# Optimization experiments

Hardware: AMD Instinct MI355X
Metric: run time of the kernel (lower is better)

The kernel has to match this reference:

```python
import jax, jax.numpy as jnp
import numpy as np
from jax import lax

# norse LIF/LI default parameters
DT = 0.001
TAU_SYN_INV = 200.0   # 1/5e-3
TAU_MEM_INV = 100.0   # 1/1e-2
V_TH = 1.0
V_LEAK = 0.0
V_RESET = 0.0
ALPHA = 100.0         # SuperSpike surrogate slope (method='super')
SEQ_LEN = 40          # LIFConstantCurrentEncoder(40)
SCALE = 50.0

@jax.custom_vjp
def heaviside(x):
    # forward: spike if x > 0; backward: SuperSpike surrogate
    return (x > 0).astype(x.dtype)

def _h_fwd(x):
    return (x > 0).astype(x.dtype), x

def _h_bwd(x, g):
    return (g / (ALPHA * jnp.abs(x) + 1.0) ** 2,)

heaviside.defvjp(_h_fwd, _h_bwd)

def constant_current_encode(current):
    # LIF membrane driven by a constant input current; emit spike train (T, B, F)
    def step(v, _):
        v = v + DT * TAU_MEM_INV * ((V_LEAK - v) + current)
        z = heaviside(v - V_TH)
        v = (1.0 - z) * v  # reset to zero on spike
        return v, z
    _, spikes = lax.scan(step, jnp.zeros_like(current), None, length=SEQ_LEN)
    return spikes

def setup_inputs() -> dict:
    key = jax.random.key(0)
    k1, k2, k3, k4 = jax.random.split(key, 4)
    batch, state_dim, hidden, out = 65536, 4, 128, 2
    x = jax.random.normal(k1, (batch, state_dim), jnp.float32)
    s_in = np.float32(np.sqrt(1.0 / (2 * state_dim)))
    s_hid = np.float32(np.sqrt(1.0 / hidden))
    w_in = jax.random.normal(k2, (hidden, 2 * state_dim), jnp.float32) * s_in   # LIFCell input weights
    w_rec = jax.random.normal(k3, (hidden, hidden), jnp.float32) * s_hid        # LIFCell recurrent weights
    w_out = jax.random.normal(k4, (out, hidden), jnp.float32) * s_hid           # LICell readout weights
    return {"x": x, "w_in": w_in, "w_rec": w_rec, "w_out": w_out}

def reference(x, w_in, w_rec, w_out):
    # encode positive / negative parts of the (scaled) observation into spikes
    x_pos = constant_current_encode(jax.nn.relu(SCALE * x))   # (T, B, 4)
    x_neg = constant_current_encode(jax.nn.relu(-SCALE * x))  # (T, B, 4)
    spikes = jnp.concatenate([x_pos, x_neg], axis=2)          # (T, B, 8)

    B = x.shape[0]
    H = w_in.shape[0]
    O = w_out.shape[0]
    z0 = jnp.zeros((B, H), x.dtype)
    v0 = jnp.zeros((B, H), x.dtype)
    i0 = jnp.zeros((B, H), x.dtype)
    vo0 = jnp.zeros((B, O), x.dtype)
    io0 = jnp.zeros((B, O), x.dtype)

    def step(carry, xt):
        z, v, i, vo, io = carry
        # --- LIFCell (recurrent spiking layer) ---
        i_dec = i - DT * TAU_SYN_INV * i
        v_dec = v + DT * TAU_MEM_INV * ((V_LEAK - v) + i)
        z_new = heaviside(v_dec - V_TH)
        v_new = (1.0 - z_new) * v_dec + z_new * V_RESET
        i_new = i_dec + xt @ w_in.T + z @ w_rec.T
        # dropout(p=0.5) is identity in eval mode
        # --- LICell (leaky-integrator readout) ---
        vo_new = vo + DT * TAU_MEM_INV * ((V_LEAK - vo) + io)
        io_new = io - DT * TAU_SYN_INV * io + z_new @ w_out.T
        return (z_new, v_new, i_new, vo_new, io_new), vo_new

    _, voltages = lax.scan(step, (z0, v0, i0, vo0, io0), spikes)  # (T, B, 2)
    m = jnp.max(voltages, axis=0)
    return jax.nn.softmax(m, axis=1)
```

## Files before the change

### kernel.cpp

```cpp
#include <hip/hip_runtime.h>


#pragma clang fp contract(off)

typedef float f32x4 __attribute__((ext_vector_type(4)));
typedef float f32x2 __attribute__((ext_vector_type(2)));
typedef short short8 __attribute__((ext_vector_type(8)));
typedef int int4v __attribute__((ext_vector_type(4)));

constexpr int TSTEPS = 40;

__device__ __forceinline__ unsigned rnbf(float f) {
    unsigned u = __float_as_uint(f);
    return (u + 0x7FFFu + ((u >> 16) & 1u)) & 0xFFFF0000u;
}

__device__ __forceinline__ void split2pair(float a, float b,
                                           unsigned& hi, unsigned& mi) {
    unsigned ha = rnbf(a), hb = rnbf(b);
    float ra = a - __uint_as_float(ha);
    float rb = b - __uint_as_float(hb);
    unsigned ma = rnbf(ra), mb = rnbf(rb);
    hi = (ha >> 16) | (hb & 0xFFFF0000u);
    mi = (ma >> 16) | (mb & 0xFFFF0000u);
}

__device__ __forceinline__ f32x4 mfma16(int4v a, int4v b, f32x4 c) {
    return __builtin_amdgcn_mfma_f32_16x16x32_bf16(
        __builtin_bit_cast(short8, a), __builtin_bit_cast(short8, b), c, 0, 0, 0);
}

template <int CTRL>
__device__ __forceinline__ float dpp_mov(float v) {
    return __int_as_float(
        __builtin_amdgcn_update_dpp(0, __float_as_int(v), CTRL, 0xF, 0xF, true));
}

__device__ __forceinline__ f32x2 lo2(f32x4 a) {
    return __builtin_shufflevector(a, a, 0, 1);
}
__device__ __forceinline__ f32x2 hi2(f32x4 a) {
    return __builtin_shufflevector(a, a, 2, 3);
}

__global__ __launch_bounds__(256, 3) void snn_kernel(
    const float* __restrict__ x,
    const float* __restrict__ w_in,
    const float* __restrict__ w_rec,
    const float* __restrict__ w_out,
    float* __restrict__ out)
{
    __shared__ char zraw[8192];

    const int tid = threadIdx.x;
    const int l   = tid & 63;
    const int wv  = tid >> 6;
    const int cl  = l & 15;
    const int kg  = l >> 4;
    const int kb  = kg * 8;
    const int b0  = blockIdx.x * 16;
    const int Ns  = wv * 32;

    const f32x2 P1  = {0.1f, 0.1f};
    const f32x2 P02 = {0.2f, 0.2f};

    int4v BrecHi[2][4], BrecMi[2][4];
#pragma unroll
    for (int t = 0; t < 2; ++t) {
        int n = Ns + t * 16 + cl;
#pragma unroll
        for (int kc = 0; kc < 4; ++kc) {
            const float* wp = w_rec + n * 128 + kc * 32 + kb;
            float4 wa = *reinterpret_cast<const float4*>(wp);
            float4 wb = *reinterpret_cast<const float4*>(wp + 4);
            float w8[8] = {wa.x, wa.y, wa.z, wa.w, wb.x, wb.y, wb.z, wb.w};
#pragma unroll
            for (int r = 0; r < 4; ++r) {
                unsigned h, m;
                split2pair(w8[2 * r], w8[2 * r + 1], h, m);
                BrecHi[t][kc][r] = (int)h;
                BrecMi[t][kc][r] = (int)m;
            }
        }
    }

    int4v BwinPk[2];
#pragma unroll
    for (int t = 0; t < 2; ++t) {
        int n = Ns + t * 16 + cl;
        float w8[8];
#pragma unroll
        for (int j = 0; j < 8; ++j)
            w8[j] = (kg < 2) ? w_in[n * 8 + j] : 0.0f;
#pragma unroll
        for (int r = 0; r < 4; ++r) {
            unsigned h, m;
            split2pair(w8[2 * r], w8[2 * r + 1], h, m);
            BwinPk[t][r] = (int)(kg == 0 ? h : (kg == 1 ? m : 0u));
        }
    }

    int4v Bwout[4];
    {
        int  ch   = cl & 1;
        int  part = (cl >> 1) & 1;
        bool act  = cl < 4;
#pragma unroll
        for (int kc = 0; kc < 4; ++kc) {
            float w8[8];
#pragma unroll
            for (int j = 0; j < 8; ++j)
                w8[j] = act ? w_out[ch * 128 + kc * 32 + kb + j] : 0.0f;
#pragma unroll
            for (int r = 0; r < 4; ++r) {
                unsigned h, m;
                split2pair(w8[2 * r], w8[2 * r + 1], h, m);
                Bwout[kc][r] = (int)(part ? m : h);
            }
        }
    }

    float xv0 = x[(size_t)(b0 + (l >> 3)) * 4 + (l & 3)];
    float xv1 = x[(size_t)(b0 + 8 + (l >> 3)) * 4 + (l & 3)];
    float s0 = 50.0f * xv0, s1 = 50.0f * xv1;
    f32x2 cur;
    cur[0] = (l & 4) ? fmaxf(-s0, 0.0f) : fmaxf(s0, 0.0f);
    cur[1] = (l & 4) ? fmaxf(-s1, 0.0f) : fmaxf(s1, 0.0f);
    f32x2 ve = {0.0f, 0.0f};

    f32x2 iSl[2] = {{0,0},{0,0}}, iSh[2] = {{0,0},{0,0}};
    f32x2 vSl[2] = {{0,0},{0,0}}, vSh[2] = {{0,0},{0,0}};
    f32x2 io_l = {0,0}, io_h = {0,0}, vo_l = {0,0}, vo_h = {0,0};
    f32x4 mx = {-3e38f,-3e38f,-3e38f,-3e38f};

    unsigned awrb[2];
#pragma unroll
    for (int t = 0; t < 2; ++t) {
        int col = Ns + t * 16 + cl;
        awrb[t] = (unsigned)((kg * 1024 + col * 2) ^ ((kg & 1) << 6));
    }
    unsigned ard = (unsigned)((cl * 256 + kg * 16) ^ ((cl & 7) << 4)) | 4096u;

    auto loadfrags = [&](int4v* zf) {
#pragma unroll
        for (int kc = 0; kc < 4; ++kc)
            zf[kc] = *reinterpret_cast<int4v*>(&zraw[ard ^ (unsigned)(kc << 6)]);
    };

    auto readout = [&](const int4v* zf) {
        f32x4 cro = {0,0,0,0};
#pragma unroll
        for (int kc = 0; kc < 4; ++kc) cro = mfma16(zf[kc], Bwout[kc], cro);
        f32x4 cr;
#pragma unroll
        for (int r = 0; r < 4; ++r) cr[r] = cro[r] + dpp_mov<0x4E>(cro[r]);
        f32x2 t2l = io_l - vo_l;
        f32x2 t2h = io_h - vo_h;
        f32x2 vnl = vo_l + P1 * t2l;
        f32x2 vnh = vo_h + P1 * t2h;
        io_l = (io_l - P02 * io_l) + lo2(cr);
        io_h = (io_h - P02 * io_h) + hi2(cr);
        vo_l = vnl;
        vo_h = vnh;
        mx[0] = fmaxf(mx[0], vnl[0]);
        mx[1] = fmaxf(mx[1], vnl[1]);
        mx[2] = fmaxf(mx[2], vnh[0]);
        mx[3] = fmaxf(mx[3], vnh[1]);
    };

    auto encoder_lif = [&](bool with_rec, const int4v* zf) {
        f32x2 te = cur - ve;
        f32x2 vv = ve + P1 * te;
        bool e0 = vv[0] > 1.0f, e1 = vv[1] > 1.0f;
        unsigned long long bm0 = __ballot(e0), bm1 = __ballot(e1);
        ve[0] = e0 ? 0.0f : vv[0];
        ve[1] = e1 ? 0.0f : vv[1];
        unsigned long long src = (cl < 8) ? (bm0 >> (cl * 8)) : (bm1 >> ((cl - 8) * 8));
        unsigned byt = (l < 32) ? ((unsigned)src & 0xFFu) : 0u;
        int4v axt;
        axt[0] = (int)(((byt & 1u)   ? 0x3F80u : 0u) | ((byt & 2u)   ? 0x3F800000u : 0u));
        axt[1] = (int)(((byt & 4u)   ? 0x3F80u : 0u) | ((byt & 8u)   ? 0x3F800000u : 0u));
        axt[2] = (int)(((byt & 16u)  ? 0x3F80u : 0u) | ((byt & 32u)  ? 0x3F800000u : 0u));
        axt[3] = (int)(((byt & 64u)  ? 0x3F80u : 0u) | ((byt & 128u) ? 0x3F800000u : 0u));
#pragma unroll
        for (int t = 0; t < 2; ++t) {
            f32x4 cin = {0,0,0,0};
            cin = mfma16(axt, BwinPk[t], cin);
            f32x4 crec = {0,0,0,0};
            if (with_rec) {
#pragma unroll
                for (int kc = 0; kc < 4; ++kc)
                    crec = mfma16(zf[kc], BrecMi[t][kc], crec);
#pragma unroll
                for (int kc = 0; kc < 4; ++kc)
                    crec = mfma16(zf[kc], BrecHi[t][kc], crec);
            }
            f32x2 idl = iSl[t] - P02 * iSl[t];
            f32x2 idh = iSh[t] - P02 * iSh[t];
            f32x2 ttl = iSl[t] - vSl[t];
            f32x2 tth = iSh[t] - vSh[t];
            f32x2 vdl = vSl[t] + P1 * ttl;
            f32x2 vdh = vSh[t] + P1 * tth;
#pragma unroll
            for (int r = 0; r < 4; ++r) {
                float vdr = (r < 2) ? vdl[r] : vdh[r - 2];
                bool zb = vdr > 1.0f;
                float vres = zb ? 0.0f : vdr;
                if (r == 0)      vSl[t][0] = vres;
                else if (r == 1) vSl[t][1] = vres;
                else if (r == 2) vSh[t][0] = vres;
                else             vSh[t][1] = vres;
                short zv = zb ? (short)0x3F80 : (short)0;
                unsigned a = (awrb[t] ^ (unsigned)(r << 4)) + (unsigned)(r * 256);
                *reinterpret_cast<short*>(&zraw[a]) = zv;
            }
            iSl[t] = (idl + lo2(cin)) + lo2(crec);
            iSh[t] = (idh + hi2(cin)) + hi2(crec);
        }
    };

    auto toggle = [&]() {
        ard ^= 4096u;
        awrb[0] ^= 4096u;
        awrb[1] ^= 4096u;
    };

    encoder_lif(false, nullptr);
    __syncthreads();
    toggle();

#pragma unroll 1
    for (int u = 1; u < TSTEPS; ++u) {
        int4v zf[4];
        loadfrags(zf);
        readout(zf);
        encoder_lif(true, zf);
        __syncthreads();
        toggle();
    }

    {
        int4v zf[4];
        loadfrags(zf);
        readout(zf);
    }

#pragma unroll
    for (int r = 0; r < 4; ++r) {
        float partner = dpp_mov<0xB1>(mx[r]);
        float mm = fmaxf(mx[r], partner);
        float es = expf(mx[r] - mm);
        float ep = expf(partner - mm);
        float inv = 1.0f / (es + ep);
        float pr = es * inv;
        if (cl < 2) out[(size_t)(b0 + kg * 4 + r) * 2 + cl] = pr;
    }
}

extern "C" void kernel_launch(void* const* d_in, const int* in_sizes, int n_in,
                              void* d_out, int out_size, void* d_ws, size_t ws_size,
                              hipStream_t stream) {
    const float* x     = (const float*)d_in[0];
    const float* w_in  = (const float*)d_in[1];
    const float* w_rec = (const float*)d_in[2];
    const float* w_out = (const float*)d_in[3];
    float* out = (float*)d_out;

    int B = in_sizes[0] / 4;
    int blocks = B / 16;
    snn_kernel<<<blocks, 256, 0, stream>>>(x, w_in, w_rec, w_out, out);
}
```

Baseline: 266.5 us.

## Process two independent batch tiles per block to interleave dependent MFMA chains

Each block now handles 32 batch rows as two independent 16-row tiles (A and B) whose recurrent MFMA chains, LIF updates and readouts are interleaved in the same loop. The shared spike buffer doubles and the grid halves. This gives the scheduler independent work to hide MFMA and LDS latency, and halves the number of barriers and weight-splitting preambles per row. In exchange, register pressure roughly doubles for state, and launch bounds drop to two blocks per CU, reducing occupancy.

Result: slower. 277.4 us (+4.1%).

```diff
diff --git a/kernel.cpp b/kernel.cpp
--- a/kernel.cpp
+++ b/kernel.cpp
@@ -43,14 +43,14 @@
     return __builtin_shufflevector(a, a, 2, 3);
 }
 
-__global__ __launch_bounds__(256, 3) void snn_kernel(
+__global__ __launch_bounds__(256, 2) void snn_kernel(
     const float* __restrict__ x,
     const float* __restrict__ w_in,
     const float* __restrict__ w_rec,
     const float* __restrict__ w_out,
     float* __restrict__ out)
 {
-    __shared__ char zraw[8192];
+    __shared__ char zraw[16384];
 
     const int tid = threadIdx.x;
     const int l   = tid & 63;
@@ -58,7 +58,7 @@
     const int cl  = l & 15;
     const int kg  = l >> 4;
     const int kb  = kg * 8;
-    const int b0  = blockIdx.x * 16;
+    const int b0  = blockIdx.x * 32;
     const int Ns  = wv * 32;
 
     const f32x2 P1  = {0.1f, 0.1f};
@@ -122,16 +122,25 @@
 
     float xv0 = x[(size_t)(b0 + (l >> 3)) * 4 + (l & 3)];
     float xv1 = x[(size_t)(b0 + 8 + (l >> 3)) * 4 + (l & 3)];
+    float xv2 = x[(size_t)(b0 + 16 + (l >> 3)) * 4 + (l & 3)];
+    float xv3 = x[(size_t)(b0 + 24 + (l >> 3)) * 4 + (l & 3)];
     float s0 = 50.0f * xv0, s1 = 50.0f * xv1;
-    f32x2 cur;
-    cur[0] = (l & 4) ? fmaxf(-s0, 0.0f) : fmaxf(s0, 0.0f);
-    cur[1] = (l & 4) ? fmaxf(-s1, 0.0f) : fmaxf(s1, 0.0f);
-    f32x2 ve = {0.0f, 0.0f};
-
-    f32x2 iSl[2] = {{0,0},{0,0}}, iSh[2] = {{0,0},{0,0}};
-    f32x2 vSl[2] = {{0,0},{0,0}}, vSh[2] = {{0,0},{0,0}};
-    f32x2 io_l = {0,0}, io_h = {0,0}, vo_l = {0,0}, vo_h = {0,0};
-    f32x4 mx = {-3e38f,-3e38f,-3e38f,-3e38f};
+    float s2 = 50.0f * xv2, s3 = 50.0f * xv3;
+    f32x2 curA, curB;
+    curA[0] = (l & 4) ? fmaxf(-s0, 0.0f) : fmaxf(s0, 0.0f);
+    curA[1] = (l & 4) ? fmaxf(-s1, 0.0f) : fmaxf(s1, 0.0f);
+    curB[0] = (l & 4) ? fmaxf(-s2, 0.0f) : fmaxf(s2, 0.0f);
+    curB[1] = (l & 4) ? fmaxf(-s3, 0.0f) : fmaxf(s3, 0.0f);
+    f32x2 veA = {0.0f, 0.0f}, veB = {0.0f, 0.0f};
+
+    f32x2 iSlA[2] = {{0,0},{0,0}}, iShA[2] = {{0,0},{0,0}};
+    f32x2 vSlA[2] = {{0,0},{0,0}}, vShA[2] = {{0,0},{0,0}};
+    f32x2 iSlB[2] = {{0,0},{0,0}}, iShB[2] = {{0,0},{0,0}};
+    f32x2 vSlB[2] = {{0,0},{0,0}}, vShB[2] = {{0,0},{0,0}};
+    f32x2 ioA_l = {0,0}, ioA_h = {0,0}, voA_l = {0,0}, voA_h = {0,0};
+    f32x2 ioB_l = {0,0}, ioB_h = {0,0}, voB_l = {0,0}, voB_h = {0,0};
+    f32x4 mxA = {-3e38f,-3e38f,-3e38f,-3e38f};
+    f32x4 mxB = {-3e38f,-3e38f,-3e38f,-3e38f};
 
     unsigned awrb[2];
 #pragma unroll
@@ -139,42 +148,61 @@
         int col = Ns + t * 16 + cl;
         awrb[t] = (unsigned)((kg * 1024 + col * 2) ^ ((kg & 1) << 6));
     }
-    unsigned ard = (unsigned)((cl * 256 + kg * 16) ^ ((cl & 7) << 4)) | 4096u;
-
-    auto loadfrags = [&](int4v* zf) {
-#pragma unroll
-        for (int kc = 0; kc < 4; ++kc)
-            zf[kc] = *reinterpret_cast<int4v*>(&zraw[ard ^ (unsigned)(kc << 6)]);
-    };
-
-    auto readout = [&](const int4v* zf) {
-        f32x4 cro = {0,0,0,0};
-#pragma unroll
-        for (int kc = 0; kc < 4; ++kc) cro = mfma16(zf[kc], Bwout[kc], cro);
-        f32x4 cr;
-#pragma unroll
-        for (int r = 0; r < 4; ++r) cr[r] = cro[r] + dpp_mov<0x4E>(cro[r]);
-        f32x2 t2l = io_l - vo_l;
-        f32x2 t2h = io_h - vo_h;
-        f32x2 vnl = vo_l + P1 * t2l;
-        f32x2 vnh = vo_h + P1 * t2h;
-        io_l = (io_l - P02 * io_l) + lo2(cr);
-        io_h = (io_h - P02 * io_h) + hi2(cr);
-        vo_l = vnl;
-        vo_h = vnh;
-        mx[0] = fmaxf(mx[0], vnl[0]);
-        mx[1] = fmaxf(mx[1], vnl[1]);
-        mx[2] = fmaxf(mx[2], vnh[0]);
-        mx[3] = fmaxf(mx[3], vnh[1]);
-    };
-
-    auto encoder_lif = [&](bool with_rec, const int4v* zf) {
-        f32x2 te = cur - ve;
-        f32x2 vv = ve + P1 * te;
-        bool e0 = vv[0] > 1.0f, e1 = vv[1] > 1.0f;
-        unsigned long long bm0 = __ballot(e0), bm1 = __ballot(e1);
-        ve[0] = e0 ? 0.0f : vv[0];
-        ve[1] = e1 ? 0.0f : vv[1];
+    unsigned ard = (unsigned)((cl * 256 + kg * 16) ^ ((cl & 7) << 4)) | 8192u;
+
+    auto loadfrags = [&](int4v* zfA, int4v* zfB) {
+#pragma unroll
+        for (int kc = 0; kc < 4; ++kc) {
+            unsigned a = ard ^ (unsigned)(kc << 6);
+            zfA[kc] = *reinterpret_cast<int4v*>(&zraw[a]);
+            zfB[kc] = *reinterpret_cast<int4v*>(&zraw[a ^ 4096u]);
+        }
+    };
+
+    auto readout = [&](const int4v* zfA, const int4v* zfB) {
+        f32x4 croA = {0,0,0,0}, croB = {0,0,0,0};
+#pragma unroll
+        for (int kc = 0; kc < 4; ++kc) {
+            croA = mfma16(zfA[kc], Bwout[kc], croA);
+            croB = mfma16(zfB[kc], Bwout[kc], croB);
+        }
+        f32x4 crA, crB;
+#pragma unroll
+        for (int r = 0; r < 4; ++r) {
+            crA[r] = croA[r] + dpp_mov<0x4E>(croA[r]);
+            crB[r] = croB[r] + dpp_mov<0x4E>(croB[r]);
+        }
+        {
+            f32x2 t2l = ioA_l - voA_l;
+            f32x2 t2h = ioA_h - voA_h;
+            f32x2 vnl = voA_l + P1 * t2l;
+            f32x2 vnh = voA_h + P1 * t2h;
+            ioA_l = (ioA_l - P02 * ioA_l) + lo2(crA);
+            ioA_h = (ioA_h - P02 * ioA_h) + hi2(crA);
+            voA_l = vnl;
+            voA_h = vnh;
+            mxA[0] = fmaxf(mxA[0], vnl[0]);
+            mxA[1] = fmaxf(mxA[1], vnl[1]);
+            mxA[2] = fmaxf(mxA[2], vnh[0]);
+            mxA[3] = fmaxf(mxA[3], vnh[1]);
+        }
+        {
+            f32x2 t2l = ioB_l - voB_l;
+            f32x2 t2h = ioB_h - voB_h;
+            f32x2 vnl = voB_l + P1 * t2l;
+            f32x2 vnh = voB_h + P1 * t2h;
+            ioB_l = (ioB_l - P02 * ioB_l) + lo2(crB);
+            ioB_h = (ioB_h - P02 * ioB_h) + hi2(crB);
+            voB_l = vnl;
+            voB_h = vnh;
+            mxB[0] = fmaxf(mxB[0], vnl[0]);
+            mxB[1] = fmaxf(mxB[1], vnl[1]);
+            mxB[2] = fmaxf(mxB[2], vnh[0]);
+            mxB[3] = fmaxf(mxB[3], vnh[1]);
+        }
+    };
+
+    auto make_axt = [&](unsigned long long bm0, unsigned long long bm1) {
         unsigned long long src = (cl < 8) ? (bm0 >> (cl * 8)) : (bm1 >> ((cl - 8) * 8));
         unsigned byt = (l < 32) ? ((unsigned)src & 0xFFu) : 0u;
         int4v axt;
@@ -182,78 +210,135 @@
         axt[1] = (int)(((byt & 4u)   ? 0x3F80u : 0u) | ((byt & 8u)   ? 0x3F800000u : 0u));
         axt[2] = (int)(((byt & 16u)  ? 0x3F80u : 0u) | ((byt & 32u)  ? 0x3F800000u : 0u));
         axt[3] = (int)(((byt & 64u)  ? 0x3F80u : 0u) | ((byt & 128u) ? 0x3F800000u : 0u));
+        return axt;
+    };
+
+    auto encoder_lif = [&](bool with_rec, const int4v* zfA, const int4v* zfB) {
+        f32x2 teA = curA - veA;
+        f32x2 vvA = veA + P1 * teA;
+        f32x2 teB = curB - veB;
+        f32x2 vvB = veB + P1 * teB;
+        bool e0 = vvA[0] > 1.0f, e1 = vvA[1] > 1.0f;
+        bool e2 = vvB[0] > 1.0f, e3 = vvB[1] > 1.0f;
+        unsigned long long bm0A = __ballot(e0), bm1A = __ballot(e1);
+        unsigned long long bm0B = __ballot(e2), bm1B = __ballot(e3);
+        veA[0] = e0 ? 0.0f : vvA[0];
+        veA[1] = e1 ? 0.0f : vvA[1];
+        veB[0] = e2 ? 0.0f : vvB[0];
+        veB[1] = e3 ? 0.0f : vvB[1];
+        int4v axtA = make_axt(bm0A, bm1A);
+        int4v axtB = make_axt(bm0B, bm1B);
 #pragma unroll
         for (int t = 0; t < 2; ++t) {
-            f32x4 cin = {0,0,0,0};
-            cin = mfma16(axt, BwinPk[t], cin);
-            f32x4 crec = {0,0,0,0};
+            f32x4 cinA = {0,0,0,0}, cinB = {0,0,0,0};
+            cinA = mfma16(axtA, BwinPk[t], cinA);
+            cinB = mfma16(axtB, BwinPk[t], cinB);
+            f32x4 crecA = {0,0,0,0}, crecB = {0,0,0,0};
             if (with_rec) {
 #pragma unroll
-                for (int kc = 0; kc < 4; ++kc)
-                    crec = mfma16(zf[kc], BrecMi[t][kc], crec);
-#pragma unroll
-                for (int kc = 0; kc < 4; ++kc)
-                    crec = mfma16(zf[kc], BrecHi[t][kc], crec);
-            }
-            f32x2 idl = iSl[t] - P02 * iSl[t];
-            f32x2 idh = iSh[t] - P02 * iSh[t];
-            f32x2 ttl = iSl[t] - vSl[t];
-            f32x2 tth = iSh[t] - vSh[t];
-            f32x2 vdl = vSl[t] + P1 * ttl;
-            f32x2 vdh = vSh[t] + P1 * tth;
-#pragma unroll
-            for (int r = 0; r < 4; ++r) {
-                float vdr = (r < 2) ? vdl[r] : vdh[r - 2];
-                bool zb = vdr > 1.0f;
-                float vres = zb ? 0.0f : vdr;
-                if (r == 0)      vSl[t][0] = vres;
-                else if (r == 1) vSl[t][1] = vres;
-                else if (r == 2) vSh[t][0] = vres;
-                else             vSh[t][1] = vres;
-                short zv = zb ? (short)0x3F80 : (short)0;
-                unsigned a = (awrb[t] ^ (unsigned)(r << 4)) + (unsigned)(r * 256);
-                *reinterpret_cast<short*>(&zraw[a]) = zv;
-            }
-            iSl[t] = (idl + lo2(cin)) + lo2(crec);
-            iSh[t] = (idh + hi2(cin)) + hi2(crec);
+                for (int kc = 0; kc < 4; ++kc) {
+                    crecA = mfma16(zfA[kc], BrecMi[t][kc], crecA);
+                    crecB = mfma16(zfB[kc], BrecMi[t][kc], crecB);
+                }
+#pragma unroll
+                for (int kc = 0; kc < 4; ++kc) {
+                    crecA = mfma16(zfA[kc], BrecHi[t][kc], crecA);
+                    crecB = mfma16(zfB[kc], BrecHi[t][kc], crecB);
+                }
+            }
+            {
+                f32x2 idl = iSlA[t] - P02 * iSlA[t];
+                f32x2 idh = iShA[t] - P02 * iShA[t];
+                f32x2 ttl = iSlA[t] - vSlA[t];
+                f32x2 tth = iShA[t] - vShA[t];
+                f32x2 vdl = vSlA[t] + P1 * ttl;
+                f32x2 vdh = vShA[t] + P1 * tth;
+#pragma unroll
+                for (int r = 0; r < 4; ++r) {
+                    float vdr = (r < 2) ? vdl[r] : vdh[r - 2];
+                    bool zb = vdr > 1.0f;
+                    float vres = zb ? 0.0f : vdr;
+                    if (r == 0)      vSlA[t][0] = vres;
+                    else if (r == 1) vSlA[t][1] = vres;
+                    else if (r == 2) vShA[t][0] = vres;
+                    else             vShA[t][1] = vres;
+                    short zv = zb ? (short)0x3F80 : (short)0;
+                    unsigned a = (awrb[t] ^ (unsigned)(r << 4)) + (unsigned)(r * 256);
+                    *reinterpret_cast<short*>(&zraw[a]) = zv;
+                }
+                iSlA[t] = (idl + lo2(cinA)) + lo2(crecA);
+                iShA[t] = (idh + hi2(cinA)) + hi2(crecA);
+            }
+            {
+                f32x2 idl = iSlB[t] - P02 * iSlB[t];
+                f32x2 idh = iShB[t] - P02 * iShB[t];
+                f32x2 ttl = iSlB[t] - vSlB[t];
+                f32x2 tth = iShB[t] - vShB[t];
+                f32x2 vdl = vSlB[t] + P1 * ttl;
+                f32x2 vdh = vShB[t] + P1 * tth;
+#pragma unroll
+                for (int r = 0; r < 4; ++r) {
+                    float vdr = (r < 2) ? vdl[r] : vdh[r - 2];
+                    bool zb = vdr > 1.0f;
+                    float vres = zb ? 0.0f : vdr;
+                    if (r == 0)      vSlB[t][0] = vres;
+                    else if (r == 1) vSlB[t][1] = vres;
+                    else if (r == 2) vShB[t][0] = vres;
+                    else             vShB[t][1] = vres;
+                    short zv = zb ? (short)0x3F80 : (short)0;
+                    unsigned a = ((awrb[t] ^ (unsigned)(r << 4)) + (unsigned)(r * 256)) ^ 4096u;
+                    *reinterpret_cast<short*>(&zraw[a]) = zv;
+                }
+                iSlB[t] = (idl + lo2(cinB)) + lo2(crecB);
+                iShB[t] = (idh + hi2(cinB)) + hi2(crecB);
+            }
         }
     };
 
     auto toggle = [&]() {
-        ard ^= 4096u;
-        awrb[0] ^= 4096u;
-        awrb[1] ^= 4096u;
-    };
-
-    encoder_lif(false, nullptr);
+        ard ^= 8192u;
+        awrb[0] ^= 8192u;
+        awrb[1] ^= 8192u;
+    };
+
+    encoder_lif(false, nullptr, nullptr);
     __syncthreads();
     toggle();
 
 #pragma unroll 1
     for (int u = 1; u < TSTEPS; ++u) {
-        int4v zf[4];
-        loadfrags(zf);
-        readout(zf);
-        encoder_lif(true, zf);
+        int4v zfA[4], zfB[4];
+        loadfrags(zfA, zfB);
+        readout(zfA, zfB);
+        encoder_lif(true, zfA, zfB);
         __syncthreads();
         toggle();
     }
 
     {
-        int4v zf[4];
-        loadfrags(zf);
-        readout(zf);
+        int4v zfA[4], zfB[4];
+        loadfrags(zfA, zfB);
+        readout(zfA, zfB);
     }
 
 #pragma unroll
     for (int r = 0; r < 4; ++r) {
-        float partner = dpp_mov<0xB1>(mx[r]);
-        float mm = fmaxf(mx[r], partner);
-        float es = expf(mx[r] - mm);
-        float ep = expf(partner - mm);
-        float inv = 1.0f / (es + ep);
-        float pr = es * inv;
-        if (cl < 2) out[(size_t)(b0 + kg * 4 + r) * 2 + cl] = pr;
+        {
+            float partner = dpp_mov<0xB1>(mxA[r]);
+            float mm = fmaxf(mxA[r], partner);
+            float es = expf(mxA[r] - mm);
+            float ep = expf(partner - mm);
+            float pr = es / (es + ep);
+            if (cl < 2) out[(size_t)(b0 + kg * 4 + r) * 2 + cl] = pr;
+        }
+        {
+            float partner = dpp_mov<0xB1>(mxB[r]);
+            float mm = fmaxf(mxB[r], partner);
+            float es = expf(mxB[r] - mm);
+            float ep = expf(partner - mm);
+            float pr = es / (es + ep);
+            if (cl < 2) out[(size_t)(b0 + 16 + kg * 4 + r) * 2 + cl] = pr;
+        }
     }
 }
 
@@ -267,6 +352,6 @@
     float* out = (float*)d_out;
 
     int B = in_sizes[0] / 4;
-    int blocks = B / 16;
+    int blocks = B / 32;
     snn_kernel<<<blocks, 256, 0, stream>>>(x, w_in, w_rec, w_out, out);
 }
```

## Precompute encoder spike masks in one wave and restrict readout to one wave

Applied to the files above, without the earlier changes.

The input encoder LIF recurrence was computed redundantly by all four waves every timestep. Now a single designated wave, rotated per block, runs all 40 encoder steps up front and stores the ballot masks in shared memory, which the per-step loop reads back. The readout MFMA, the max tracking and the final softmax store now run only in that designated wave instead of all four. This removes duplicated VALU and MFMA work per step, at the cost of a serial prologue in one wave, an extra barrier and load imbalance across waves.

After: 245.4 us. -7.9%, faster.

```diff
diff --git a/kernel.cpp b/kernel.cpp
--- a/kernel.cpp
+++ b/kernel.cpp
@@ -51,6 +51,7 @@
     float* __restrict__ out)
 {
     __shared__ char zraw[8192];
+    __shared__ __align__(16) unsigned long long msk[TSTEPS][2];
 
     const int tid = threadIdx.x;
     const int l   = tid & 63;
@@ -60,6 +61,7 @@
     const int kb  = kg * 8;
     const int b0  = blockIdx.x * 16;
     const int Ns  = wv * 32;
+    const int des = blockIdx.x & 3;
 
     const f32x2 P1  = {0.1f, 0.1f};
     const f32x2 P02 = {0.2f, 0.2f};
@@ -120,13 +122,24 @@
         }
     }
 
-    float xv0 = x[(size_t)(b0 + (l >> 3)) * 4 + (l & 3)];
-    float xv1 = x[(size_t)(b0 + 8 + (l >> 3)) * 4 + (l & 3)];
-    float s0 = 50.0f * xv0, s1 = 50.0f * xv1;
-    f32x2 cur;
-    cur[0] = (l & 4) ? fmaxf(-s0, 0.0f) : fmaxf(s0, 0.0f);
-    cur[1] = (l & 4) ? fmaxf(-s1, 0.0f) : fmaxf(s1, 0.0f);
-    f32x2 ve = {0.0f, 0.0f};
+    if (wv == des) {
+        float xv0 = x[(size_t)(b0 + (l >> 3)) * 4 + (l & 3)];
+        float xv1 = x[(size_t)(b0 + 8 + (l >> 3)) * 4 + (l & 3)];
+        float s0 = 50.0f * xv0, s1 = 50.0f * xv1;
+        f32x2 cur, ve = {0.0f, 0.0f};
+        cur[0] = (l & 4) ? fmaxf(-s0, 0.0f) : fmaxf(s0, 0.0f);
+        cur[1] = (l & 4) ? fmaxf(-s1, 0.0f) : fmaxf(s1, 0.0f);
+#pragma unroll 1
+        for (int u = 0; u < TSTEPS; ++u) {
+            f32x2 te = cur - ve;
+            f32x2 vv = ve + P1 * te;
+            bool e0 = vv[0] > 1.0f, e1 = vv[1] > 1.0f;
+            unsigned long long bm0 = __ballot(e0), bm1 = __ballot(e1);
+            ve[0] = e0 ? 0.0f : vv[0];
+            ve[1] = e1 ? 0.0f : vv[1];
+            if (l == 0) { msk[u][0] = bm0; msk[u][1] = bm1; }
+        }
+    }
 
     f32x2 iSl[2] = {{0,0},{0,0}}, iSh[2] = {{0,0},{0,0}};
     f32x2 vSl[2] = {{0,0},{0,0}}, vSh[2] = {{0,0},{0,0}};
@@ -168,13 +181,9 @@
         mx[3] = fmaxf(mx[3], vnh[1]);
     };
 
-    auto encoder_lif = [&](bool with_rec, const int4v* zf) {
-        f32x2 te = cur - ve;
-        f32x2 vv = ve + P1 * te;
-        bool e0 = vv[0] > 1.0f, e1 = vv[1] > 1.0f;
-        unsigned long long bm0 = __ballot(e0), bm1 = __ballot(e1);
-        ve[0] = e0 ? 0.0f : vv[0];
-        ve[1] = e1 ? 0.0f : vv[1];
+    auto encoder_lif = [&](int u, bool with_rec, const int4v* zf) {
+        unsigned long long bm0 = msk[u][0];
+        unsigned long long bm1 = msk[u][1];
         unsigned long long src = (cl < 8) ? (bm0 >> (cl * 8)) : (bm1 >> ((cl - 8) * 8));
         unsigned byt = (l < 32) ? ((unsigned)src & 0xFFu) : 0u;
         int4v axt;
@@ -184,6 +193,7 @@
         axt[3] = (int)(((byt & 64u)  ? 0x3F80u : 0u) | ((byt & 128u) ? 0x3F800000u : 0u));
 #pragma unroll
         for (int t = 0; t < 2; ++t) {
+            f32x2 idl, idh, ttl, tth, vdl, vdh;
             f32x4 cin = {0,0,0,0};
             cin = mfma16(axt, BwinPk[t], cin);
             f32x4 crec = {0,0,0,0};
@@ -195,12 +205,12 @@
                 for (int kc = 0; kc < 4; ++kc)
                     crec = mfma16(zf[kc], BrecHi[t][kc], crec);
             }
-            f32x2 idl = iSl[t] - P02 * iSl[t];
-            f32x2 idh = iSh[t] - P02 * iSh[t];
-            f32x2 ttl = iSl[t] - vSl[t];
-            f32x2 tth = iSh[t] - vSh[t];
-            f32x2 vdl = vSl[t] + P1 * ttl;
-            f32x2 vdh = vSh[t] + P1 * tth;
+            idl = iSl[t] - P02 * iSl[t];
+            idh = iSh[t] - P02 * iSh[t];
+            ttl = iSl[t] - vSl[t];
+            tth = iSh[t] - vSh[t];
+            vdl = vSl[t] + P1 * ttl;
+            vdh = vSh[t] + P1 * tth;
 #pragma unroll
             for (int r = 0; r < 4; ++r) {
                 float vdr = (r < 2) ? vdl[r] : vdh[r - 2];
@@ -225,7 +235,8 @@
         awrb[1] ^= 4096u;
     };
 
-    encoder_lif(false, nullptr);
+    __syncthreads();
+    encoder_lif(0, false, nullptr);
     __syncthreads();
     toggle();
 
@@ -233,27 +244,26 @@
     for (int u = 1; u < TSTEPS; ++u) {
         int4v zf[4];
         loadfrags(zf);
-        readout(zf);
-        encoder_lif(true, zf);
+        if (wv == des) readout(zf);
+        encoder_lif(u, true, zf);
         __syncthreads();
         toggle();
     }
 
-    {
+    if (wv == des) {
         int4v zf[4];
         loadfrags(zf);
         readout(zf);
-    }
-
-#pragma unroll
-    for (int r = 0; r < 4; ++r) {
-        float partner = dpp_mov<0xB1>(mx[r]);
-        float mm = fmaxf(mx[r], partner);
-        float es = expf(mx[r] - mm);
-        float ep = expf(partner - mm);
-        float inv = 1.0f / (es + ep);
-        float pr = es * inv;
-        if (cl < 2) out[(size_t)(b0 + kg * 4 + r) * 2 + cl] = pr;
+#pragma unroll
+        for (int r = 0; r < 4; ++r) {
+            float partner = dpp_mov<0xB1>(mx[r]);
+            float mm = fmaxf(mx[r], partner);
+            float es = expf(mx[r] - mm);
+            float ep = expf(partner - mm);
+            float inv = 1.0f / (es + ep);
+            float pr = es * inv;
+            if (cl < 2) out[(size_t)(b0 + kg * 4 + r) * 2 + cl] = pr;
+        }
     }
 }
 
```
